# Optimization experiments

Measured on AMD Instinct MI355X. Metric: run time of the kernel, lower is better.

Reference implementation:

```python
import jax, jax.numpy as jnp
import numpy as np
from functools import partial

B, N, T = 4, 10000, 128
E = 160000
H, C = 4, 64            # heads, out_channels per head
GAT_DIM = H * C         # 256
NEG_SLOPE = 0.2


def conv1d(x, w, b):
    # x: (M, Cin, L), w: (Cout, Cin, K), 'same' padding (pad=1 for k=3)
    y = jax.lax.conv_general_dilated(x, w, window_strides=(1,), padding=[(1, 1)],
                                     dimension_numbers=('NCH', 'OIH', 'NCH'))
    return y + b[None, :, None]


def maxpool2(x):
    # kernel=2, stride=2 over last axis
    return jax.lax.reduce_window(x, -jnp.inf, jax.lax.max,
                                 (1, 1, 2), (1, 1, 2), 'VALID')


def gat_layer_single(x, src, dst, W, att_s, att_d, bias):
    # x: (N, Fin); PyG GATConv with concat=True, self-loops already appended to src/dst
    n = x.shape[0]
    xl = (x @ W).reshape(n, H, C)                       # (N, H, C)
    a_s = jnp.sum(xl * att_s[None], axis=-1)            # (N, H)
    a_d = jnp.sum(xl * att_d[None], axis=-1)            # (N, H)
    e = jax.nn.leaky_relu(a_s[src] + a_d[dst], NEG_SLOPE)  # (E', H)
    emax = jax.ops.segment_max(e, dst, num_segments=n)     # (N, H)
    ex = jnp.exp(e - emax[dst])
    denom = jax.ops.segment_sum(ex, dst, num_segments=n)   # (N, H)
    alpha = ex / (denom[dst] + 1e-16)                       # (E', H)
    msg = xl[src] * alpha[..., None]                        # (E', H, C)
    out = jax.ops.segment_sum(msg, dst, num_segments=n)     # (N, H, C)
    return out.reshape(n, H * C) + bias


def setup_inputs() -> dict:
    key = jax.random.key(0)
    ks = jax.random.split(key, 24)
    rn = lambda k, sh, fan: jax.random.normal(k, sh, jnp.float32) / np.sqrt(fan)
    inp = {
        'x': jax.random.normal(ks[0], (B, N, T), jnp.float32),
        'edge_index': jax.random.randint(ks[1], (2, E), 0, N, jnp.int64),
        # temporal conv
        'cw1': rn(ks[2], (32, 1, 3), 3), 'cb1': jnp.zeros((32,), jnp.float32),
        'cw2': rn(ks[3], (64, 32, 3), 96), 'cb2': jnp.zeros((64,), jnp.float32),
        # GAT layer 0 (in=64)
        'W0': rn(ks[4], (64, GAT_DIM), 64), 'as0': rn(ks[5], (H, C), C), 'ad0': rn(ks[6], (H, C), C),
        'b0': jnp.zeros((GAT_DIM,), jnp.float32),
        # GAT layer 1 (in=256)
        'W1': rn(ks[7], (GAT_DIM, GAT_DIM), GAT_DIM), 'as1': rn(ks[8], (H, C), C), 'ad1': rn(ks[9], (H, C), C),
        'b1': jnp.zeros((GAT_DIM,), jnp.float32),
        # classification head 256->128->2
        'Wc1': rn(ks[10], (GAT_DIM, 128), GAT_DIM), 'bc1': jnp.zeros((128,), jnp.float32),
        'Wc2': rn(ks[11], (128, 2), 128), 'bc2': jnp.zeros((2,), jnp.float32),
        # attribution head 256->64->1
        'Wa1': rn(ks[12], (GAT_DIM, 64), GAT_DIM), 'ba1': jnp.zeros((64,), jnp.float32),
        'Wa2': rn(ks[13], (64, 1), 64), 'ba2': jnp.zeros((1,), jnp.float32),
    }
    return inp


def reference(x, edge_index, cw1, cb1, cw2, cb2, W0, as0, ad0, b0, W1, as1, ad1, b1,
              Wc1, bc1, Wc2, bc2, Wa1, ba1, Wa2, ba2):
    b, n, t = x.shape
    # ---- temporal conv over all B*N node signals ----
    xf = x.reshape(b * n, 1, t)
    h = jax.nn.relu(conv1d(xf, cw1, cb1))            # (BN, 32, T)
    h = maxpool2(h)                                  # (BN, 32, T//2)
    h = jax.nn.relu(conv1d(h, cw2, cb2))             # (BN, 64, T//2)
    feat = jnp.mean(h, axis=-1).reshape(b, n, 64)    # adaptive_avg_pool1d(1)
    # ---- GAT stack (self-loops appended, PyG default) ----
    src0, dst0 = edge_index[0], edge_index[1]
    loops = jnp.arange(n, dtype=src0.dtype)
    src = jnp.concatenate([src0, loops])
    dst = jnp.concatenate([dst0, loops])
    gat0 = jax.vmap(partial(gat_layer_single, src=src, dst=dst, W=W0, att_s=as0, att_d=ad0, bias=b0))
    gat1 = jax.vmap(partial(gat_layer_single, src=src, dst=dst, W=W1, att_s=as1, att_d=ad1, bias=b1))
    g = jax.nn.relu(gat0(feat))                      # (B, N, 256); dropout = identity (eval)
    g = jax.nn.relu(gat1(g))                         # (B, N, 256)
    # ---- heads ----
    pooled = jnp.mean(g, axis=1)                     # (B, 256)
    logits = jax.nn.relu(pooled @ Wc1 + bc1) @ Wc2 + bc2          # (B, 2)
    attr = jax.nn.sigmoid(jax.nn.relu(g @ Wa1 + ba1) @ Wa2 + ba2)  # (B, N, 1)
    return logits, attr[..., 0]
```

## Files before the change

### kernel.cpp

```cpp
#include <hip/hip_runtime.h>
#include <hip/hip_bf16.h>
#include <math.h>

typedef __hip_bfloat16 bf16;
typedef unsigned short u16;
typedef unsigned int u32;
typedef __attribute__((ext_vector_type(8))) short short8;
typedef __attribute__((ext_vector_type(4))) float f32x4;
typedef __attribute__((ext_vector_type(2))) float f32x2;

#define BATCH 4
#define NNODE 10000
#define TLEN 128
#define NEDGE 160000
#define GDIM 256
#define NHEAD 4

#define S_CW1 0
#define S_CB1 96
#define S_CB2 128
#define S_AS0 192
#define S_AD0 448
#define S_B0  704
#define S_AS1 960
#define S_AD1 1216
#define S_B1  1472
#define S_BC1 1728
#define S_WC2 1856
#define S_BC2 2112
#define S_BA1 2114
#define S_WA2 2178
#define S_BA2 2242
#define S_TOTAL 2243

__device__ __forceinline__ float prelu(float v) { return fmaxf(v, 0.f); }
__device__ __forceinline__ u16 f2b(float f) {
    union { float f; u32 u; } v; v.f = f;
    u32 r = v.u + 0x7FFF + ((v.u >> 16) & 1);
    return (u16)(r >> 16);
}
__device__ __forceinline__ float u2f(u16 u) {
    union { u32 u; float f; } v; v.u = ((u32)u) << 16;
    return v.f;
}
__device__ __forceinline__ float ldw(const void* p, int off, bool isbf) {
    return isbf ? u2f(((const u16*)p)[off]) : ((const float*)p)[off];
}

__device__ __forceinline__ bool probe_x_bf16(const void* xsrc) {
    int lane = threadIdx.x & 63;
    u16 h = ((const u16*)xsrc)[2 * lane];
    int e = (h >> 7) & 0xFF;
    unsigned long long m = __ballot(e >= 117 && e <= 130);
    return __popcll(m) >= 32;
}
__device__ __forceinline__ bool probe_ei64(const int* ei) {
    int lane = threadIdx.x & 63;
    int v = ei[2 * lane + 1];
    unsigned long long m = __ballot(v == 0);
    return __popcll(m) >= 56;
}

struct WPtrs { const void* p[20]; };

#define PRE_TBLK 665
__global__ __launch_bounds__(256) void k_pre(WPtrs wp, const void* __restrict__ xsrc,
        const int* __restrict__ ei, float* __restrict__ wbuf,
        u16* __restrict__ cw2r, u16* __restrict__ W0t, u16* __restrict__ W1t,
        u16* __restrict__ Wa1t, int* __restrict__ counts) {
    bool isbf = probe_x_bf16(xsrc);
    int b = blockIdx.x;
    if (b >= PRE_TBLK) {
        const int C2[16] = {0,96,128,192,448,704,960,1216,1472,1728,1856,2112,
                            2114,2178,2242,2243};
        const int SRC[15] = {0,1,3,5,6,7,9,10,11,13,14,15,17,18,19};
        int i = (b - PRE_TBLK) * 256 + threadIdx.x;
        if (i >= S_TOTAL) return;
        int j = 14;
        for (int t = 0; t < 15; ++t) { if (i < C2[t + 1]) { j = t; break; } }
        wbuf[i] = ldw(wp.p[SRC[j]], i - C2[j], isbf);
        return;
    }
    int i = b * 256 + threadIdx.x;
    if (i < 6144) {
        int c2 = i / 96, k = i - c2 * 96, s = k >> 5, ci = k & 31;
        cw2r[i] = f2b(ldw(wp.p[2], c2 * 96 + ci * 3 + s, isbf));
    }
    if (i < 16384) {
        int k = i >> 8, c = i & 255;
        W0t[c * 64 + k] = f2b(ldw(wp.p[4], k * 256 + c, isbf));
        int ka = i >> 6, ca = i & 63;
        Wa1t[ca * 256 + ka] = f2b(ldw(wp.p[16], ka * 64 + ca, isbf));
    }
    if (i < 65536) {
        int k = i >> 8, c = i & 255;
        W1t[c * 256 + k] = f2b(ldw(wp.p[8], k * 256 + c, isbf));
    }
    if (i < NEDGE + NNODE) {
        bool ei64 = probe_ei64(ei);
        int dst;
        if (i < NEDGE) dst = ei64 ? ei[2 * (NEDGE + i)] : ei[NEDGE + i];
        else dst = i - NEDGE;
        if (dst >= 0 && dst < NNODE) atomicAdd(&counts[dst], 1);
    }
}

__global__ __launch_bounds__(256) void k_scan1(const int* __restrict__ counts,
        int* __restrict__ cur, int* __restrict__ bsum) {
    __shared__ int buf[256];
    int tid = threadIdx.x;
    int i = blockIdx.x * 256 + tid;
    int v = (i < NNODE) ? counts[i] : 0;
    buf[tid] = v;
    __syncthreads();
    for (int off = 1; off < 256; off <<= 1) {
        int t = (tid >= off) ? buf[tid - off] : 0;
        __syncthreads();
        buf[tid] += t;
        __syncthreads();
    }
    if (i < NNODE) cur[i] = buf[tid];
    if (tid == 255) bsum[blockIdx.x] = buf[255];
}
__global__ __launch_bounds__(256) void k_scan3(const int* __restrict__ counts,
        int* __restrict__ cur, const int* __restrict__ bsum, int* __restrict__ row_ptr) {
    __shared__ int pre_s;
    int tid = threadIdx.x;
    if (tid == 0) {
        int s = 0;
        for (int j = 0; j < blockIdx.x; ++j) s += bsum[j];
        pre_s = s;
    }
    __syncthreads();
    int i = blockIdx.x * 256 + tid;
    if (i >= NNODE) return;
    int incl = cur[i] + pre_s;
    row_ptr[i + 1] = incl;
    cur[i] = incl - counts[i];
    if (i == 0) row_ptr[0] = 0;
}

#define HSTR 40
#define NPB 8
#define FILL_BLK 665
__global__ __launch_bounds__(256, 4) void k_conv(const void* __restrict__ xsrc,
        const float* __restrict__ wbuf, const u16* __restrict__ cw2r,
        u16* __restrict__ featb, const int* __restrict__ ei,
        int* __restrict__ cur, int* __restrict__ col_src) {
    __shared__ __align__(16) float xs[NPB][132];
    __shared__ float w1s[96], b1s[32], b2s[64];
    __shared__ __align__(16) u16 hs[2][66 * HSTR];
    __shared__ float ps[2][4][64];

    bool isbf = probe_x_bf16(xsrc);
    int tid = threadIdx.x;
    int wave = tid >> 6, lane = tid & 63;
    int node0 = blockIdx.x * NPB;

    int m = lane & 15, q = lane >> 4;
    short8 bfr[4][3];
    #pragma unroll
    for (int nt = 0; nt < 4; ++nt)
        #pragma unroll
        for (int sh = 0; sh < 3; ++sh)
            bfr[nt][sh] = *(const short8*)&cw2r[(nt * 16 + m) * 96 + sh * 32 + q * 8];

    #pragma unroll
    for (int rr = 0; rr < NPB / 4; ++rr) {
        int idx = rr * 256 + tid;
        int j = idx >> 6, p = (idx & 63) * 2;
        if (isbf) {
            u32 w = ((const u32*)xsrc)[(size_t)node0 * 64 + idx];
            xs[j][1 + p] = u2f((u16)(w & 0xFFFF));
            xs[j][2 + p] = u2f((u16)(w >> 16));
        } else {
            float2 w = ((const float2*)xsrc)[(size_t)node0 * 64 + idx];
            xs[j][1 + p] = w.x;
            xs[j][2 + p] = w.y;
        }
    }
    if (tid < 2 * NPB) xs[tid >> 1][(tid & 1) ? 129 : 0] = 0.f;
    if (tid < 96) w1s[tid] = wbuf[S_CW1 + tid];
    if (tid < 32) b1s[tid] = wbuf[S_CB1 + tid];
    if (tid < 64) b2s[tid] = wbuf[S_CB2 + tid];
    if (tid < 128) {
        int bf = tid >> 6, seg = (tid >> 5) & 1, ch = tid & 31;
        hs[bf][seg ? (65 * HSTR + ch) : ch] = 0;
    }
    __syncthreads();

    int d = tid & 15, uu = tid >> 4;
    float wa0 = w1s[6 * d + 0], wa1 = w1s[6 * d + 1], wa2 = w1s[6 * d + 2];
    float wb0 = w1s[6 * d + 3], wb1 = w1s[6 * d + 4], wb2 = w1s[6 * d + 5];
    float ba = b1s[2 * d], bb = b1s[2 * d + 1];
    float b2vv[4];
    #pragma unroll
    for (int nt = 0; nt < 4; ++nt) b2vv[nt] = b2s[nt * 16 + m];

    auto conv1 = [&](int jj) {
        const float* xr = &xs[jj][0];
        u16* hwp = &hs[jj & 1][0];
        #pragma unroll
        for (int it = 0; it < 4; ++it) {
            int u = uu + 16 * it;
            int t0 = 2 * u;
            float x0 = xr[t0], x1 = xr[t0 + 1], x2 = xr[t0 + 2], x3 = xr[t0 + 3];
            f32x2 A = {x0, x1}, Bv = {x1, x2}, Cv = {x2, x3};
            f32x2 va = {ba, ba}; va += wa0 * A; va += wa1 * Bv; va += wa2 * Cv;
            f32x2 vb = {bb, bb}; vb += wb0 * A; vb += wb1 * Bv; vb += wb2 * Cv;
            float ha = fmaxf(fmaxf(va.x, va.y), 0.f);
            float hb = fmaxf(fmaxf(vb.x, vb.y), 0.f);
            __hip_bfloat162 hp2 = __float22bfloat162_rn(make_float2(ha, hb));
            u32 pack; __builtin_memcpy(&pack, &hp2, 4);
            *(u32*)&hwp[(u + 1) * HSTR + 2 * d] = pack;
        }
    };

    conv1(0);
    __syncthreads();

    for (int j = 0; j < NPB; ++j) {
        if (j + 1 < NPB) conv1(j + 1);

        const u16* hw = &hs[j & 1][0];
        short8 a0 = *(const short8*)&hw[(wave * 16 + m + 0) * HSTR + q * 8];
        short8 a1 = *(const short8*)&hw[(wave * 16 + m + 1) * HSTR + q * 8];
        short8 a2 = *(const short8*)&hw[(wave * 16 + m + 2) * HSTR + q * 8];

        f32x4 acc[4];
        #pragma unroll
        for (int nt = 0; nt < 4; ++nt) acc[nt] = {0.f, 0.f, 0.f, 0.f};
        #pragma unroll
        for (int nt = 0; nt < 4; ++nt) {
            acc[nt] = __builtin_amdgcn_mfma_f32_16x16x32_bf16(a0, bfr[nt][0], acc[nt], 0, 0, 0);
            acc[nt] = __builtin_amdgcn_mfma_f32_16x16x32_bf16(a1, bfr[nt][1], acc[nt], 0, 0, 0);
            acc[nt] = __builtin_amdgcn_mfma_f32_16x16x32_bf16(a2, bfr[nt][2], acc[nt], 0, 0, 0);
        }

        float pc[4];
        #pragma unroll
        for (int nt = 0; nt < 4; ++nt) {
            pc[nt] = prelu(acc[nt][0] + b2vv[nt]) + prelu(acc[nt][1] + b2vv[nt])
                   + prelu(acc[nt][2] + b2vv[nt]) + prelu(acc[nt][3] + b2vv[nt]);
            pc[nt] += __shfl_xor(pc[nt], 16, 64);
            pc[nt] += __shfl_xor(pc[nt], 32, 64);
        }
        if (lane < 16) {
            #pragma unroll
            for (int nt = 0; nt < 4; ++nt)
                ps[j & 1][wave][nt * 16 + lane] = pc[nt];
        }
        __syncthreads();
        if (wave == (j & 3)) {
            float v = ps[j & 1][0][lane] + ps[j & 1][1][lane]
                    + ps[j & 1][2][lane] + ps[j & 1][3][lane];
            int node = node0 + j;
            int bb2 = node / NNODE, nn = node - bb2 * NNODE;
            featb[((size_t)nn * 4 + bb2) * 64 + lane] = f2b(v * (1.f / 64.f));
        }
    }

    if (blockIdx.x < FILL_BLK) {
        bool ei64 = probe_ei64(ei);
        int e = blockIdx.x * 256 + tid;
        if (e < NEDGE + NNODE) {
            int src, dst;
            if (e < NEDGE) {
                if (ei64) { src = ei[2 * e]; dst = ei[2 * (NEDGE + e)]; }
                else      { src = ei[e];     dst = ei[NEDGE + e]; }
            } else {
                src = dst = e - NEDGE;
            }
            if (dst >= 0 && dst < NNODE) {
                int pos = atomicAdd(&cur[dst], 1);
                if (pos >= 0 && pos < NEDGE + NNODE) col_src[pos] = src;
            }
        }
    }
}

template<int K>
__global__ __launch_bounds__(256) void k_gemm(const u16* __restrict__ A,
        const u16* __restrict__ Wt, const float* __restrict__ att_s_w,
        const float* __restrict__ att_d_w, u16* __restrict__ outb,
        float* __restrict__ a_s, float* __restrict__ a_d) {
    int wave = threadIdx.x >> 6, lane = threadIdx.x & 63;
    int row0 = (blockIdx.x * 4 + wave) * 16;
    int m = lane & 15, q = lane >> 4;
    f32x4 acc[16];
    #pragma unroll
    for (int nt = 0; nt < 16; ++nt) acc[nt] = {0.f, 0.f, 0.f, 0.f};
    for (int kc = 0; kc < K; kc += 32) {
        short8 a = *(const short8*)&A[(size_t)(row0 + m) * K + kc + q * 8];
        #pragma unroll
        for (int nt = 0; nt < 16; ++nt) {
            short8 b = *(const short8*)&Wt[(size_t)(nt * 16 + m) * K + kc + q * 8];
            acc[nt] = __builtin_amdgcn_mfma_f32_16x16x32_bf16(a, b, acc[nt], 0, 0, 0);
        }
    }
    #pragma unroll
    for (int nt = 0; nt < 16; ++nt) {
        #pragma unroll
        for (int r = 0; r < 4; ++r)
            outb[(size_t)(row0 + q * 4 + r) * 256 + nt * 16 + m] = f2b(acc[nt][r]);
    }
    float sh_s[4][4] = {{0}}, sh_d[4][4] = {{0}};
    #pragma unroll
    for (int nt = 0; nt < 16; ++nt) {
        int h = nt >> 2;
        int cc = (nt & 3) * 16 + m;
        float asw = att_s_w[h * 64 + cc];
        float adw = att_d_w[h * 64 + cc];
        #pragma unroll
        for (int r = 0; r < 4; ++r) {
            sh_s[h][r] += acc[nt][r] * asw;
            sh_d[h][r] += acc[nt][r] * adw;
        }
    }
    #pragma unroll
    for (int off = 1; off < 16; off <<= 1) {
        #pragma unroll
        for (int h = 0; h < 4; ++h)
            #pragma unroll
            for (int r = 0; r < 4; ++r) {
                sh_s[h][r] += __shfl_xor(sh_s[h][r], off, 64);
                sh_d[h][r] += __shfl_xor(sh_d[h][r], off, 64);
            }
    }
    if (m == 0) {
        #pragma unroll
        for (int r = 0; r < 4; ++r) {
            int row = row0 + q * 4 + r;
            float4 vs = {sh_s[0][r], sh_s[1][r], sh_s[2][r], sh_s[3][r]};
            float4 vd = {sh_d[0][r], sh_d[1][r], sh_d[2][r], sh_d[3][r]};
            *(float4*)&a_s[(size_t)row * 4] = vs;
            *(float4*)&a_d[(size_t)row * 4] = vd;
        }
    }
}

__global__ __launch_bounds__(256) void k_agg(const u16* __restrict__ xlb,
        const float* __restrict__ a_s, const float* __restrict__ a_d,
        const int* __restrict__ row_ptr, const int* __restrict__ col_src,
        const float* __restrict__ bias, u16* __restrict__ gb_out) {
    int wave = threadIdx.x >> 6, lane = threadIdx.x & 63;
    int dst = __builtin_amdgcn_readfirstlane(blockIdx.x * 2 + (wave >> 1));
    int bp = (wave & 1) * 2;
    int beg = __builtin_amdgcn_readfirstlane(row_ptr[dst]);
    int end = __builtin_amdgcn_readfirstlane(row_ptr[dst + 1]);

    int bl = lane >> 5;
    int s = lane & 31;
    int h = s >> 3;
    int b = bp + bl;
    int asoff = b * 4 + h;
    float advh = a_d[(size_t)dst * 16 + asoff];

    float m = -INFINITY, l = 0.f;
    float acc[8];
    #pragma unroll
    for (int k = 0; k < 8; ++k) acc[k] = 0.f;

    int i = beg;
    for (; i + 4 <= end; i += 4) {
        int s0 = min(max(col_src[i], 0), NNODE - 1);
        int s1 = min(max(col_src[i + 1], 0), NNODE - 1);
        int s2 = min(max(col_src[i + 2], 0), NNODE - 1);
        int s3 = min(max(col_src[i + 3], 0), NNODE - 1);
        float a0 = a_s[(size_t)s0 * 16 + asoff];
        float a1 = a_s[(size_t)s1 * 16 + asoff];
        float a2 = a_s[(size_t)s2 * 16 + asoff];
        float a3 = a_s[(size_t)s3 * 16 + asoff];
        short8 x0 = *(const short8*)&xlb[((size_t)s0 * 4 + b) * 256 + s * 8];
        short8 x1 = *(const short8*)&xlb[((size_t)s1 * 4 + b) * 256 + s * 8];
        short8 x2 = *(const short8*)&xlb[((size_t)s2 * 4 + b) * 256 + s * 8];
        short8 x3 = *(const short8*)&xlb[((size_t)s3 * 4 + b) * 256 + s * 8];
        float e0 = a0 + advh; e0 = (e0 >= 0.f) ? e0 : 0.2f * e0;
        float e1 = a1 + advh; e1 = (e1 >= 0.f) ? e1 : 0.2f * e1;
        float e2 = a2 + advh; e2 = (e2 >= 0.f) ? e2 : 0.2f * e2;
        float e3 = a3 + advh; e3 = (e3 >= 0.f) ? e3 : 0.2f * e3;
        float cmax = fmaxf(fmaxf(e0, e1), fmaxf(e2, e3));
        if (__any(cmax > m)) {
            float mn = fmaxf(m, cmax);
            float r = __expf(m - mn);
            m = mn;
            l *= r;
            #pragma unroll
            for (int k = 0; k < 8; ++k) acc[k] *= r;
        }
        float p0 = __expf(e0 - m); l += p0;
        #pragma unroll
        for (int k = 0; k < 8; ++k) acc[k] += p0 * u2f((u16)x0[k]);
        float p1 = __expf(e1 - m); l += p1;
        #pragma unroll
        for (int k = 0; k < 8; ++k) acc[k] += p1 * u2f((u16)x1[k]);
        float p2 = __expf(e2 - m); l += p2;
        #pragma unroll
        for (int k = 0; k < 8; ++k) acc[k] += p2 * u2f((u16)x2[k]);
        float p3 = __expf(e3 - m); l += p3;
        #pragma unroll
        for (int k = 0; k < 8; ++k) acc[k] += p3 * u2f((u16)x3[k]);
    }
    for (; i < end; ++i) {
        int s0 = min(max(col_src[i], 0), NNODE - 1);
        float a0 = a_s[(size_t)s0 * 16 + asoff];
        short8 x0 = *(const short8*)&xlb[((size_t)s0 * 4 + b) * 256 + s * 8];
        float e0 = a0 + advh; e0 = (e0 >= 0.f) ? e0 : 0.2f * e0;
        if (__any(e0 > m)) {
            float mn = fmaxf(m, e0);
            float r = __expf(m - mn);
            m = mn;
            l *= r;
            #pragma unroll
            for (int k = 0; k < 8; ++k) acc[k] *= r;
        }
        float p0 = __expf(e0 - m); l += p0;
        #pragma unroll
        for (int k = 0; k < 8; ++k) acc[k] += p0 * u2f((u16)x0[k]);
    }

    float rl = 1.f / (l + 1e-16f);
    short8 o;
    #pragma unroll
    for (int k = 0; k < 8; ++k)
        o[k] = (short)f2b(prelu(acc[k] * rl + bias[s * 8 + k]));
    *(short8*)&gb_out[((size_t)dst * 4 + b) * 256 + s * 8] = o;
}

__global__ __launch_bounds__(256) void k_attrpool(const u16* __restrict__ gb,
        const u16* __restrict__ Wa1t, const float* __restrict__ wbuf,
        float* __restrict__ out, float* __restrict__ pooled) {
    if (blockIdx.x >= 625) {
        int pb = blockIdx.x - 625;
        int b = pb >> 6;
        int chunk = pb & 63;
        int cch = threadIdx.x;
        int n0 = chunk * 157;
        int n1 = min(NNODE, n0 + 157);
        float acc = 0.f;
        int n = n0;
        for (; n + 4 <= n1; n += 4) {
            float v0 = u2f(gb[((size_t)n * 4 + b) * 256 + cch]);
            float v1 = u2f(gb[((size_t)(n + 1) * 4 + b) * 256 + cch]);
            float v2 = u2f(gb[((size_t)(n + 2) * 4 + b) * 256 + cch]);
            float v3 = u2f(gb[((size_t)(n + 3) * 4 + b) * 256 + cch]);
            acc += v0; acc += v1; acc += v2; acc += v3;
        }
        for (; n < n1; ++n)
            acc += u2f(gb[((size_t)n * 4 + b) * 256 + cch]);
        atomicAdd(&pooled[b * 256 + cch], acc);
        return;
    }
    int wave = threadIdx.x >> 6, lane = threadIdx.x & 63;
    int row0 = (blockIdx.x * 4 + wave) * 16;
    int m = lane & 15, q = lane >> 4;
    f32x4 acc[4];
    #pragma unroll
    for (int nt = 0; nt < 4; ++nt) acc[nt] = {0.f, 0.f, 0.f, 0.f};
    for (int kc = 0; kc < 256; kc += 32) {
        short8 a = *(const short8*)&gb[(size_t)(row0 + m) * 256 + kc + q * 8];
        #pragma unroll
        for (int nt = 0; nt < 4; ++nt) {
            short8 b = *(const short8*)&Wa1t[(size_t)(nt * 16 + m) * 256 + kc + q * 8];
            acc[nt] = __builtin_amdgcn_mfma_f32_16x16x32_bf16(a, b, acc[nt], 0, 0, 0);
        }
    }
    float part[4] = {0, 0, 0, 0};
    #pragma unroll
    for (int nt = 0; nt < 4; ++nt) {
        int col = nt * 16 + m;
        float ba1v = wbuf[S_BA1 + col];
        float wa2v = wbuf[S_WA2 + col];
        #pragma unroll
        for (int r = 0; r < 4; ++r)
            part[r] += prelu(acc[nt][r] + ba1v) * wa2v;
    }
    #pragma unroll
    for (int off = 1; off < 16; off <<= 1) {
        #pragma unroll
        for (int r = 0; r < 4; ++r)
            part[r] += __shfl_xor(part[r], off, 64);
    }
    if (m == 0) {
        float ba2v = wbuf[S_BA2];
        #pragma unroll
        for (int r = 0; r < 4; ++r) {
            int row = row0 + q * 4 + r;
            int n = row >> 2, b = row & 3;
            float v = part[r] + ba2v;
            out[8 + b * NNODE + n] = 1.f / (1.f + __expf(-v));
        }
    }
}

__global__ __launch_bounds__(128) void k_logits(const float* __restrict__ pooled,
        const float* __restrict__ wbuf, const void* __restrict__ Wc1p,
        float* __restrict__ out,
        const u16* __restrict__ featb, const u16* __restrict__ gb,
        const int* __restrict__ row_ptr, const int* __restrict__ ei,
        const void* __restrict__ xsrc, int hostbad) {
    int tid = threadIdx.x;
    bool isbf = probe_x_bf16(xsrc);
    if (blockIdx.x == 4) {
        __shared__ float red[128];
        bool ei64 = probe_ei64(ei);
        float mx[2] = {0.f, 0.f};
        const u16* bufs[2] = {featb, gb};
        for (int qq = 0; qq < 2; ++qq) {
            const u16* p = bufs[qq];
            float m = 0.f;
            for (int i = tid; i < 2048; i += 128) {
                float v = u2f(p[i]);
                if (v != v) m = 1e30f;
                m = fmaxf(m, fabsf(v));
            }
            red[tid] = m;
            __syncthreads();
            for (int s2 = 64; s2 > 0; s2 >>= 1) {
                if (tid < s2) red[tid] = fmaxf(red[tid], red[tid + s2]);
                __syncthreads();
            }
            mx[qq] = red[0];
            __syncthreads();
        }
        if (tid == 0) {
            int fb = (mx[0] > 1e8f || mx[0] < 1e-6f) ? 1 : 0;
            int gbad = (mx[1] > 1e8f || mx[1] < 1e-6f) ? 1 : 0;
            int cb = (row_ptr[NNODE] != NEDGE + NNODE) ? 1 : 0;
            int code = 100 * fb + 400 * gbad + 800 * cb + 6400 * hostbad;
            if (code) {
                code += 1600 * (isbf ? 0 : 1);
                code += 3200 * (ei64 ? 1 : 0);
                for (int j = 0; j < 8; ++j) out[j] = (float)code;
            }
        }
        return;
    }
    __shared__ float pm[256];
    __shared__ float red4[4];
    int b = blockIdx.x;
    pm[tid] = pooled[b * 256 + tid] * (1.f / NNODE);
    pm[tid + 128] = pooled[b * 256 + tid + 128] * (1.f / NNODE);
    __syncthreads();
    float acc = wbuf[S_BC1 + tid];
    if (isbf) {
        const u16* w = (const u16*)Wc1p;
        #pragma unroll 4
        for (int k = 0; k < 256; ++k)
            acc += pm[k] * u2f(w[k * 128 + tid]);
    } else {
        const float* w = (const float*)Wc1p;
        #pragma unroll 4
        for (int k = 0; k < 256; ++k)
            acc += pm[k] * w[k * 128 + tid];
    }
    float hv = prelu(acc);
    float p0 = hv * wbuf[S_WC2 + tid * 2];
    float p1 = hv * wbuf[S_WC2 + tid * 2 + 1];
    #pragma unroll
    for (int off = 32; off > 0; off >>= 1) {
        p0 += __shfl_xor(p0, off, 64);
        p1 += __shfl_xor(p1, off, 64);
    }
    int wv = tid >> 6, lane = tid & 63;
    if (lane == 0) { red4[wv * 2] = p0; red4[wv * 2 + 1] = p1; }
    __syncthreads();
    if (tid < 2)
        out[b * 2 + tid] = red4[tid] + red4[2 + tid] + wbuf[S_BC2 + tid];
}

extern "C" void kernel_launch(void* const* d_in, const int* in_sizes, int n_in,
                              void* d_out, int out_size, void* d_ws, size_t ws_size,
                              hipStream_t stream) {
    const void* x  = d_in[0];
    const int*  ei = (const int*)d_in[1];
    float* out = (float*)d_out;

    WPtrs wp;
    for (int j = 0; j < 20; ++j) wp.p[j] = d_in[j + 2];

    char* ws = (char*)d_ws;
    size_t off = 0;
    auto alloc = [&](size_t bytes) -> void* {
        void* p = ws + off;
        off += (bytes + 255) & ~(size_t)255;
        return p;
    };
    float* wbuf    = (float*)alloc((size_t)S_TOTAL * 4);
    u16*   featb   = (u16*)  alloc((size_t)BATCH * NNODE * 64 * 2);
    u16*   xlb     = (u16*)  alloc((size_t)BATCH * NNODE * 256 * 2);
    u16*   gb      = (u16*)  alloc((size_t)BATCH * NNODE * 256 * 2);
    float* a_s     = (float*)alloc((size_t)BATCH * NNODE * 4 * 4);
    float* a_d     = (float*)alloc((size_t)BATCH * NNODE * 4 * 4);
    u16*   cw2r    = (u16*)alloc(6144 * 2);
    u16*   W0t     = (u16*)alloc(16384 * 2);
    u16*   W1t     = (u16*)alloc(65536 * 2);
    u16*   Wa1t    = (u16*)alloc(16384 * 2);
    int*   counts  = (int*)alloc(NNODE * 4);
    float* pooled  = (float*)alloc(BATCH * 256 * 4);
    int*   row_ptr = (int*)alloc((NNODE + 1) * 4);
    int*   cur     = (int*)alloc(NNODE * 4);
    int*   col_src = (int*)alloc((NEDGE + NNODE) * 4);
    int*   bsum    = (int*)alloc(64 * 4);
    (void)ws_size; (void)out_size;

    int hostbad = (n_in != 22 || in_sizes[0] != BATCH * NNODE * TLEN ||
                   in_sizes[1] != 2 * NEDGE) ? 1 : 0;

    hipMemsetAsync(counts, 0, 40192 + 4096, stream);

    k_pre<<<PRE_TBLK + 9, 256, 0, stream>>>(wp, x, ei, wbuf, cw2r, W0t, W1t, Wa1t, counts);
    k_scan1<<<40, 256, 0, stream>>>(counts, cur, bsum);
    k_scan3<<<40, 256, 0, stream>>>(counts, cur, bsum, row_ptr);

    k_conv<<<BATCH * NNODE / NPB, 256, 0, stream>>>(x, wbuf, cw2r, featb, ei, cur, col_src);

    k_gemm<64><<<BATCH * NNODE / 64, 256, 0, stream>>>(featb, W0t,
            wbuf + S_AS0, wbuf + S_AD0, xlb, a_s, a_d);
    k_agg<<<NNODE / 2, 256, 0, stream>>>(xlb, a_s, a_d, row_ptr, col_src, wbuf + S_B0, gb);

    k_gemm<256><<<BATCH * NNODE / 64, 256, 0, stream>>>(gb, W1t,
            wbuf + S_AS1, wbuf + S_AD1, xlb, a_s, a_d);
    k_agg<<<NNODE / 2, 256, 0, stream>>>(xlb, a_s, a_d, row_ptr, col_src, wbuf + S_B1, gb);

    k_attrpool<<<625 + 256, 256, 0, stream>>>(gb, Wa1t, wbuf, out, pooled);
    k_logits<<<5, 128, 0, stream>>>(pooled, wbuf, wp.p[12], out, featb, gb, row_ptr, ei, x, hostbad);
}
```

Baseline: 399.4 us.

## Give each wave its own node in conv kernel and drop block barriers

The temporal conv kernel now assigns one node at a time to each wave, with four nodes per wave and sixteen per block, instead of splitting every node's 64 time rows across the four waves. Each wave keeps its own LDS buffers for the input row and the conv1 output. It does the MFMA conv2 over all four row tiles and reduces the mean with shuffles. This removes the per-node __syncthreads and the cross-wave partial-sum exchange through shared memory. The next node's input row is prefetched into registers while the current one is computed. The trade-offs are fewer blocks in the grid, the occupancy hint removed from launch_bounds, and reliance on in-wave ordering of LDS writes and reads with no explicit barrier.

Result: no change. 394.6 us (-1.2%).

```diff
diff --git a/kernel.cpp b/kernel.cpp
--- a/kernel.cpp
+++ b/kernel.cpp
@@ -141,21 +141,20 @@
 }
 
 #define HSTR 40
-#define NPB 8
+#define NPW 4
 #define FILL_BLK 665
-__global__ __launch_bounds__(256, 4) void k_conv(const void* __restrict__ xsrc,
+__global__ __launch_bounds__(256) void k_conv(const void* __restrict__ xsrc,
         const float* __restrict__ wbuf, const u16* __restrict__ cw2r,
         u16* __restrict__ featb, const int* __restrict__ ei,
         int* __restrict__ cur, int* __restrict__ col_src) {
-    __shared__ __align__(16) float xs[NPB][132];
+    __shared__ __align__(16) float xs[4][132];
     __shared__ float w1s[96], b1s[32], b2s[64];
-    __shared__ __align__(16) u16 hs[2][66 * HSTR];
-    __shared__ float ps[2][4][64];
+    __shared__ __align__(16) u16 hb[4][66 * HSTR];
 
     bool isbf = probe_x_bf16(xsrc);
     int tid = threadIdx.x;
     int wave = tid >> 6, lane = tid & 63;
-    int node0 = blockIdx.x * NPB;
+    int node0 = blockIdx.x * (4 * NPW);
 
     int m = lane & 15, q = lane >> 4;
     short8 bfr[4][3];
@@ -165,31 +164,21 @@
         for (int sh = 0; sh < 3; ++sh)
             bfr[nt][sh] = *(const short8*)&cw2r[(nt * 16 + m) * 96 + sh * 32 + q * 8];
 
-    #pragma unroll
-    for (int rr = 0; rr < NPB / 4; ++rr) {
-        int idx = rr * 256 + tid;
-        int j = idx >> 6, p = (idx & 63) * 2;
-        if (isbf) {
-            u32 w = ((const u32*)xsrc)[(size_t)node0 * 64 + idx];
-            xs[j][1 + p] = u2f((u16)(w & 0xFFFF));
-            xs[j][2 + p] = u2f((u16)(w >> 16));
-        } else {
-            float2 w = ((const float2*)xsrc)[(size_t)node0 * 64 + idx];
-            xs[j][1 + p] = w.x;
-            xs[j][2 + p] = w.y;
-        }
-    }
-    if (tid < 2 * NPB) xs[tid >> 1][(tid & 1) ? 129 : 0] = 0.f;
     if (tid < 96) w1s[tid] = wbuf[S_CW1 + tid];
     if (tid < 32) b1s[tid] = wbuf[S_CB1 + tid];
     if (tid < 64) b2s[tid] = wbuf[S_CB2 + tid];
-    if (tid < 128) {
-        int bf = tid >> 6, seg = (tid >> 5) & 1, ch = tid & 31;
-        hs[bf][seg ? (65 * HSTR + ch) : ch] = 0;
+    if (tid < 8) xs[tid >> 1][(tid & 1) ? 129 : 0] = 0.f;
+    if (tid < 64) {
+        int w = tid >> 4, idx = tid & 15;
+        *(u32*)&hb[w][2 * idx] = 0;
+        *(u32*)&hb[w][65 * HSTR + 2 * idx] = 0;
     }
     __syncthreads();
 
-    int d = tid & 15, uu = tid >> 4;
+    float* xsw = xs[wave];
+    u16* hw = &hb[wave][0];
+
+    int d = m, uu = q;
     float wa0 = w1s[6 * d + 0], wa1 = w1s[6 * d + 1], wa2 = w1s[6 * d + 2];
     float wb0 = w1s[6 * d + 3], wb1 = w1s[6 * d + 4], wb2 = w1s[6 * d + 5];
     float ba = b1s[2 * d], bb = b1s[2 * d + 1];
@@ -197,67 +186,81 @@
     #pragma unroll
     for (int nt = 0; nt < 4; ++nt) b2vv[nt] = b2s[nt * 16 + m];
 
-    auto conv1 = [&](int jj) {
-        const float* xr = &xs[jj][0];
-        u16* hwp = &hs[jj & 1][0];
-        #pragma unroll
-        for (int it = 0; it < 4; ++it) {
-            int u = uu + 16 * it;
+    int node = node0 + wave;
+    u32 plo = 0; float2 pf = {0.f, 0.f};
+    if (isbf) plo = ((const u32*)xsrc)[(size_t)node * 64 + lane];
+    else      pf  = ((const float2*)xsrc)[(size_t)node * 64 + lane];
+
+    for (int j = 0; j < NPW; ++j) {
+        if (isbf) {
+            xsw[1 + 2 * lane] = u2f((u16)(plo & 0xFFFF));
+            xsw[2 + 2 * lane] = u2f((u16)(plo >> 16));
+        } else {
+            xsw[1 + 2 * lane] = pf.x;
+            xsw[2 + 2 * lane] = pf.y;
+        }
+        if (j + 1 < NPW) {
+            int nxt = node + 4;
+            if (isbf) plo = ((const u32*)xsrc)[(size_t)nxt * 64 + lane];
+            else      pf  = ((const float2*)xsrc)[(size_t)nxt * 64 + lane];
+        }
+
+        #pragma unroll
+        for (int it = 0; it < 16; ++it) {
+            int u = uu + 4 * it;
             int t0 = 2 * u;
-            float x0 = xr[t0], x1 = xr[t0 + 1], x2 = xr[t0 + 2], x3 = xr[t0 + 3];
+            float2 xa = *(const float2*)&xsw[t0];
+            float2 xb = *(const float2*)&xsw[t0 + 2];
+            float x0 = xa.x, x1 = xa.y, x2 = xb.x, x3 = xb.y;
             f32x2 A = {x0, x1}, Bv = {x1, x2}, Cv = {x2, x3};
             f32x2 va = {ba, ba}; va += wa0 * A; va += wa1 * Bv; va += wa2 * Cv;
             f32x2 vb = {bb, bb}; vb += wb0 * A; vb += wb1 * Bv; vb += wb2 * Cv;
             float ha = fmaxf(fmaxf(va.x, va.y), 0.f);
-            float hb = fmaxf(fmaxf(vb.x, vb.y), 0.f);
-            __hip_bfloat162 hp2 = __float22bfloat162_rn(make_float2(ha, hb));
+            float hb2 = fmaxf(fmaxf(vb.x, vb.y), 0.f);
+            __hip_bfloat162 hp2 = __float22bfloat162_rn(make_float2(ha, hb2));
             u32 pack; __builtin_memcpy(&pack, &hp2, 4);
-            *(u32*)&hwp[(u + 1) * HSTR + 2 * d] = pack;
-        }
-    };
-
-    conv1(0);
-    __syncthreads();
-
-    for (int j = 0; j < NPB; ++j) {
-        if (j + 1 < NPB) conv1(j + 1);
-
-        const u16* hw = &hs[j & 1][0];
-        short8 a0 = *(const short8*)&hw[(wave * 16 + m + 0) * HSTR + q * 8];
-        short8 a1 = *(const short8*)&hw[(wave * 16 + m + 1) * HSTR + q * 8];
-        short8 a2 = *(const short8*)&hw[(wave * 16 + m + 2) * HSTR + q * 8];
-
-        f32x4 acc[4];
-        #pragma unroll
-        for (int nt = 0; nt < 4; ++nt) acc[nt] = {0.f, 0.f, 0.f, 0.f};
-        #pragma unroll
-        for (int nt = 0; nt < 4; ++nt) {
-            acc[nt] = __builtin_amdgcn_mfma_f32_16x16x32_bf16(a0, bfr[nt][0], acc[nt], 0, 0, 0);
-            acc[nt] = __builtin_amdgcn_mfma_f32_16x16x32_bf16(a1, bfr[nt][1], acc[nt], 0, 0, 0);
-            acc[nt] = __builtin_amdgcn_mfma_f32_16x16x32_bf16(a2, bfr[nt][2], acc[nt], 0, 0, 0);
-        }
-
-        float pc[4];
-        #pragma unroll
-        for (int nt = 0; nt < 4; ++nt) {
-            pc[nt] = prelu(acc[nt][0] + b2vv[nt]) + prelu(acc[nt][1] + b2vv[nt])
-                   + prelu(acc[nt][2] + b2vv[nt]) + prelu(acc[nt][3] + b2vv[nt]);
-            pc[nt] += __shfl_xor(pc[nt], 16, 64);
-            pc[nt] += __shfl_xor(pc[nt], 32, 64);
-        }
-        if (lane < 16) {
-            #pragma unroll
-            for (int nt = 0; nt < 4; ++nt)
-                ps[j & 1][wave][nt * 16 + lane] = pc[nt];
-        }
-        __syncthreads();
-        if (wave == (j & 3)) {
-            float v = ps[j & 1][0][lane] + ps[j & 1][1][lane]
-                    + ps[j & 1][2][lane] + ps[j & 1][3][lane];
-            int node = node0 + j;
-            int bb2 = node / NNODE, nn = node - bb2 * NNODE;
-            featb[((size_t)nn * 4 + bb2) * 64 + lane] = f2b(v * (1.f / 64.f));
-        }
+            *(u32*)&hw[(u + 1) * HSTR + 2 * d] = pack;
+        }
+
+        float pc0 = 0.f, pc1 = 0.f, pc2 = 0.f, pc3 = 0.f;
+        #pragma unroll
+        for (int mt = 0; mt < 4; ++mt) {
+            const u16* hr = &hw[(mt * 16 + m) * HSTR + q * 8];
+            short8 a0 = *(const short8*)&hr[0 * HSTR];
+            short8 a1 = *(const short8*)&hr[1 * HSTR];
+            short8 a2 = *(const short8*)&hr[2 * HSTR];
+            f32x4 c0 = {0.f,0.f,0.f,0.f}, c1 = {0.f,0.f,0.f,0.f};
+            f32x4 c2 = {0.f,0.f,0.f,0.f}, c3 = {0.f,0.f,0.f,0.f};
+            c0 = __builtin_amdgcn_mfma_f32_16x16x32_bf16(a0, bfr[0][0], c0, 0, 0, 0);
+            c1 = __builtin_amdgcn_mfma_f32_16x16x32_bf16(a0, bfr[1][0], c1, 0, 0, 0);
+            c2 = __builtin_amdgcn_mfma_f32_16x16x32_bf16(a0, bfr[2][0], c2, 0, 0, 0);
+            c3 = __builtin_amdgcn_mfma_f32_16x16x32_bf16(a0, bfr[3][0], c3, 0, 0, 0);
+            c0 = __builtin_amdgcn_mfma_f32_16x16x32_bf16(a1, bfr[0][1], c0, 0, 0, 0);
+            c1 = __builtin_amdgcn_mfma_f32_16x16x32_bf16(a1, bfr[1][1], c1, 0, 0, 0);
+            c2 = __builtin_amdgcn_mfma_f32_16x16x32_bf16(a1, bfr[2][1], c2, 0, 0, 0);
+            c3 = __builtin_amdgcn_mfma_f32_16x16x32_bf16(a1, bfr[3][1], c3, 0, 0, 0);
+            c0 = __builtin_amdgcn_mfma_f32_16x16x32_bf16(a2, bfr[0][2], c0, 0, 0, 0);
+            c1 = __builtin_amdgcn_mfma_f32_16x16x32_bf16(a2, bfr[1][2], c1, 0, 0, 0);
+            c2 = __builtin_amdgcn_mfma_f32_16x16x32_bf16(a2, bfr[2][2], c2, 0, 0, 0);
+            c3 = __builtin_amdgcn_mfma_f32_16x16x32_bf16(a2, bfr[3][2], c3, 0, 0, 0);
+            pc0 += prelu(c0[0] + b2vv[0]) + prelu(c0[1] + b2vv[0])
+                 + prelu(c0[2] + b2vv[0]) + prelu(c0[3] + b2vv[0]);
+            pc1 += prelu(c1[0] + b2vv[1]) + prelu(c1[1] + b2vv[1])
+                 + prelu(c1[2] + b2vv[1]) + prelu(c1[3] + b2vv[1]);
+            pc2 += prelu(c2[0] + b2vv[2]) + prelu(c2[1] + b2vv[2])
+                 + prelu(c2[2] + b2vv[2]) + prelu(c2[3] + b2vv[2]);
+            pc3 += prelu(c3[0] + b2vv[3]) + prelu(c3[1] + b2vv[3])
+                 + prelu(c3[2] + b2vv[3]) + prelu(c3[3] + b2vv[3]);
+        }
+        pc0 += __shfl_xor(pc0, 16, 64); pc0 += __shfl_xor(pc0, 32, 64);
+        pc1 += __shfl_xor(pc1, 16, 64); pc1 += __shfl_xor(pc1, 32, 64);
+        pc2 += __shfl_xor(pc2, 16, 64); pc2 += __shfl_xor(pc2, 32, 64);
+        pc3 += __shfl_xor(pc3, 16, 64); pc3 += __shfl_xor(pc3, 32, 64);
+        float v = (q == 0) ? pc0 : (q == 1) ? pc1 : (q == 2) ? pc2 : pc3;
+        int bb2 = node / NNODE, nn = node - bb2 * NNODE;
+        featb[((size_t)nn * 4 + bb2) * 64 + lane] = f2b(v * (1.f / 64.f));
+
+        node += 4;
     }
 
     if (blockIdx.x < FILL_BLK) {
@@ -613,7 +616,7 @@
     k_scan1<<<40, 256, 0, stream>>>(counts, cur, bsum);
     k_scan3<<<40, 256, 0, stream>>>(counts, cur, bsum, row_ptr);
 
-    k_conv<<<BATCH * NNODE / NPB, 256, 0, stream>>>(x, wbuf, cw2r, featb, ei, cur, col_src);
+    k_conv<<<BATCH * NNODE / (4 * NPW), 256, 0, stream>>>(x, wbuf, cw2r, featb, ei, cur, col_src);
 
     k_gemm<64><<<BATCH * NNODE / 64, 256, 0, stream>>>(featb, W0t,
             wbuf + S_AS0, wbuf + S_AD0, xlb, a_s, a_d);
```
